# Optimization experiments

Measured on AMD Instinct MI355X. Metric: run time of the kernel, lower is better.

## Reference

```python
import jax, jax.numpy as jnp
import numpy as np

N = 20000   # nodes
E = 640000  # edges (avg degree 32)
D = 128     # feature dim
BN_EPS = 1e-5


def setup_inputs() -> dict:
    key = jax.random.key(0)
    ks = jax.random.split(key, 24)
    s = 1.0 / np.sqrt(D)
    inp = {
        'h': jax.random.normal(ks[0], (N, D), jnp.float32),
        'e': jax.random.normal(ks[1], (E, D), jnp.float32),
        'src': jax.random.randint(ks[2], (E,), 0, N, jnp.int32),
        'dst': jax.random.randint(ks[3], (E,), 0, N, jnp.int32),
        'Wa': jax.random.normal(ks[4], (D, D), jnp.float32) * s,
        'ba': jnp.zeros((D,), jnp.float32),
        'Wb': jax.random.normal(ks[5], (D, D), jnp.float32) * s,
        'bb': jnp.zeros((D,), jnp.float32),
        'Wc': jax.random.normal(ks[6], (D, D), jnp.float32) * s,
        'bc': jnp.zeros((D,), jnp.float32),
        'Wd': jax.random.normal(ks[7], (D, D), jnp.float32) * s,
        'bd': jnp.zeros((D,), jnp.float32),
        'We': jax.random.normal(ks[8], (D, D), jnp.float32) * s,
        'be': jnp.zeros((D,), jnp.float32),
        'gamma_h': jnp.ones((D,), jnp.float32),
        'beta_h': jnp.zeros((D,), jnp.float32),
        'mean_h': jax.random.normal(ks[9], (D,), jnp.float32) * 0.1,
        'var_h': jax.random.uniform(ks[10], (D,), jnp.float32) + 0.5,
        'gamma_e': jnp.ones((D,), jnp.float32),
        'beta_e': jnp.zeros((D,), jnp.float32),
        'mean_e': jax.random.normal(ks[11], (D,), jnp.float32) * 0.1,
        'var_e': jax.random.uniform(ks[12], (D,), jnp.float32) + 0.5,
    }
    return inp


def reference(h, e, src, dst, Wa, ba, Wb, bb, Wc, bc, Wd, bd, We, be,
              gamma_h, beta_h, mean_h, var_h, gamma_e, beta_e, mean_e, var_e):
    # Node/edge linear projections (same as Linear: x @ W.T + b)
    Ah = h @ Wa.T + ba
    Bh = h @ Wb.T + bb
    Dh = h @ Wd.T + bd
    Eh = h @ We.T + be
    Ce = e @ Wc.T + bc

    # Edge gate: e_ij = Ce + Dh[src] + Eh[dst]
    e_new = Ce + Dh[src] + Eh[dst]          # [E, D]
    sigma = jax.nn.sigmoid(e_new)           # [E, D]

    # Normalized gated aggregation over incoming edges at each destination node
    num = jax.ops.segment_sum(sigma * Bh[src], dst, num_segments=N)  # [N, D]
    den = jax.ops.segment_sum(sigma, dst, num_segments=N)            # [N, D]
    h_new = Ah + num / (den + 1e-6)

    # BatchNorm (inference form, as written in the torch forward) + ReLU
    h_out = jax.nn.relu(gamma_h * (h_new - mean_h) / jnp.sqrt(var_h + BN_EPS) + beta_h)
    e_out = jax.nn.relu(gamma_e * (e_new - mean_e) / jnp.sqrt(var_e + BN_EPS) + beta_e)
    return h_out, e_out
```

## Files before the change

kernel.cpp:

```cpp
#include <hip/hip_runtime.h>

#define NN 20000
#define NE 640000
#define DIM 128
#define ND (NN * DIM)

typedef float f32x4 __attribute__((ext_vector_type(4)));
typedef __bf16 bf16x4 __attribute__((ext_vector_type(4)));
typedef __bf16 bf16x8 __attribute__((ext_vector_type(8)));
typedef unsigned int u32;
typedef u32 u32x2 __attribute__((ext_vector_type(2)));

__device__ __forceinline__ int swz(int r, int c) {
  return r * DIM + (c ^ ((r & 7) << 3));
}
__device__ __forceinline__ int sgaddr(int row, int col) {
  return row * DIM + ((col + ((row & 12) << 1)) & 127);
}
__device__ __forceinline__ u32 pk_bf16(float a, float b) {
  return __builtin_amdgcn_perm(__float_as_uint(b), __float_as_uint(a), 0x07060302u);
}
__device__ __forceinline__ float bf16_lo(u32 w) { return __uint_as_float(w << 16); }
__device__ __forceinline__ float bf16_hi(u32 w) { return __uint_as_float(w & 0xffff0000u); }

__global__ void prep(const float* __restrict__ Wa, const float* __restrict__ Wb,
                     const float* __restrict__ Wd, const float* __restrict__ We,
                     const float* __restrict__ Wc, __bf16* __restrict__ wbf,
                     __bf16* __restrict__ wcp,
                     const float* __restrict__ gh, const float* __restrict__ bh,
                     const float* __restrict__ mh, const float* __restrict__ vh,
                     const float* __restrict__ ge, const float* __restrict__ be_,
                     const float* __restrict__ me, const float* __restrict__ ve,
                     float* __restrict__ bn) {
  int b = blockIdx.x;
  int tid = threadIdx.x;
  if (b < 256) {
    int g = b * 256 + tid;
    int m = g >> 14;
    int off = g & 16383;
    const float* s = (m == 0) ? Wa : (m == 1) ? Wb : (m == 2) ? Wd : We;
    wbf[g] = (__bf16)s[off];
    if (g < DIM) {
      float sc = gh[g] * rsqrtf(vh[g] + 1e-5f);
      bn[g] = sc;
      bn[DIM + g] = bh[g] - mh[g] * sc;
    } else if (g < 2 * DIM) {
      int c = g - DIM;
      float sc = ge[c] * rsqrtf(ve[c] + 1e-5f);
      bn[2 * DIM + c] = sc;
      bn[3 * DIM + c] = be_[c] - me[c] * sc;
    }
  } else {
    int t2 = (b - 256) * 256 + tid;
    int lane = t2 & 63, nt = (t2 >> 6) & 7, ks = t2 >> 9;
    int lq = lane >> 4, lm = lane & 15;
    const float* srcp = Wc + (nt * 16 + lm) * DIM + ks * 32 + lq * 8;
    bf16x8 v;
#pragma unroll
    for (int j = 0; j < 8; ++j) v[j] = (__bf16)srcp[j];
    *(bf16x8*)(wcp + t2 * 8) = v;
  }
}

__global__ void hist(const int* __restrict__ dst, int* __restrict__ cur) {
  int e = blockIdx.x * 256 + threadIdx.x;
  if (e < NE) atomicAdd(cur + dst[e], 1);
}

__global__ __launch_bounds__(1024) void scan20k(int* __restrict__ cur) {
  __shared__ int wsum[16];
  int tid = threadIdx.x, wid = tid >> 6, lane = tid & 63;
  int carry = 0;
  for (int base = 0; base < NN; base += 4096) {
    int idx = base + tid * 4;
    int4 v = {0, 0, 0, 0};
    if (idx < NN) v = *(const int4*)(cur + idx);
    int sum = v.x + v.y + v.z + v.w;
    int x = sum;
#pragma unroll
    for (int d = 1; d < 64; d <<= 1) {
      int y = __shfl_up(x, d, 64);
      if (lane >= d) x += y;
    }
    if (lane == 63) wsum[wid] = x;
    __syncthreads();
    if (tid < 16) {
      int s = wsum[tid];
#pragma unroll
      for (int d = 1; d < 16; d <<= 1) {
        int y = __shfl_up(s, d, 64);
        if (tid >= d) s += y;
      }
      wsum[tid] = s;
    }
    __syncthreads();
    int excl = carry + ((wid > 0) ? wsum[wid - 1] : 0) + x - sum;
    if (idx < NN) {
      int4 o;
      o.x = excl; o.y = excl + v.x; o.z = o.y + v.y; o.w = o.z + v.z;
      *(int4*)(cur + idx) = o;
    }
    carry += wsum[15];
    __syncthreads();
  }
}

__global__ void scatter(const int* __restrict__ dst, int* __restrict__ cur,
                        int* __restrict__ perm) {
  int e = blockIdx.x * 256 + threadIdx.x;
  if (e < NE) {
    int p = atomicAdd(cur + dst[e], 1);
    perm[p] = e;
  }
}

__global__ __launch_bounds__(256) void node_gemm(
    const float* __restrict__ h, const __bf16* __restrict__ wbf,
    const float* __restrict__ ba, const float* __restrict__ bb,
    const float* __restrict__ bd, const float* __restrict__ be,
    const float* __restrict__ bc,
    float* __restrict__ Ah, __bf16* __restrict__ Bhb,
    __bf16* __restrict__ Dhb, __bf16* __restrict__ Ehb) {
  __shared__ __bf16 As[64 * DIM];
  __shared__ __bf16 Ws[DIM * DIM];
  const int tid = threadIdx.x;
  const int m = blockIdx.x & 3;
  const int row0 = (blockIdx.x >> 2) * 64;

#pragma unroll
  for (int it = 0; it < 8; ++it) {
    int flat = it * 1024 + tid * 4;
    int r = flat >> 7, c = flat & 127;
    int grow = row0 + r;
    f32x4 v = (f32x4){0.f, 0.f, 0.f, 0.f};
    if (grow < NN) v = *(const f32x4*)(h + grow * DIM + c);
    u32x2 pk;
    pk[0] = pk_bf16(v[0], v[1]);
    pk[1] = pk_bf16(v[2], v[3]);
    *(u32x2*)(As + swz(r, c)) = pk;
  }
#pragma unroll
  for (int it = 0; it < 8; ++it) {
    int chunk = it * 256 + tid;
    int r = chunk >> 4, c0 = (chunk & 15) << 3;
    bf16x8 v = *(const bf16x8*)(wbf + m * DIM * DIM + (chunk << 3));
    *(bf16x8*)(Ws + swz(r, c0)) = v;
  }
  __syncthreads();

  const int wv = tid >> 6, lane = tid & 63;
  const int lq = lane >> 4, lm = lane & 15;

  f32x4 acc[8];
#pragma unroll
  for (int i = 0; i < 8; ++i) acc[i] = (f32x4){0.f, 0.f, 0.f, 0.f};
#pragma unroll
  for (int ks = 0; ks < 4; ++ks) {
    int k0 = ks * 32 + lq * 8;
    int ar = wv * 16 + lm;
    bf16x8 a = *(const bf16x8*)(As + swz(ar, k0));
#pragma unroll
    for (int nt = 0; nt < 8; ++nt) {
      int bcol = nt * 16 + lm;
      bf16x8 b = *(const bf16x8*)(Ws + swz(bcol, k0));
      acc[nt] = __builtin_amdgcn_mfma_f32_16x16x32_bf16(a, b, acc[nt], 0, 0, 0);
    }
  }

  const float* bias = (m == 0) ? ba : (m == 1) ? bb : (m == 2) ? bd : be;
#pragma unroll
  for (int nt = 0; nt < 8; ++nt) {
    int col = nt * 16 + lm;
    float bv = bias[col];
    if (m == 2) bv += bc[col];
#pragma unroll
    for (int r = 0; r < 4; ++r) {
      int grow = row0 + wv * 16 + lq * 4 + r;
      if (grow < NN) {
        float val = acc[nt][r] + bv;
        if (m == 0) Ah[grow * DIM + col] = val;
        else if (m == 1) Bhb[grow * DIM + col] = (__bf16)val;
        else if (m == 2) Dhb[grow * DIM + col] = (__bf16)val;
        else Ehb[grow * DIM + col] = (__bf16)val;
      }
    }
  }
}

union SmemU {
  __bf16 As[64 * DIM];
  u32 sgp[64 * DIM];
};

__global__ __launch_bounds__(256, 4) void edge_gemm(
    const float* __restrict__ e, const __bf16* __restrict__ wcp,
    const int* __restrict__ src, const int* __restrict__ dst,
    const int* __restrict__ perm,
    const __bf16* __restrict__ Bhb, const __bf16* __restrict__ Dhb,
    const __bf16* __restrict__ Ehb,
    float* __restrict__ num, float* __restrict__ den,
    float* __restrict__ e_out, const float* __restrict__ bn) {
  __shared__ SmemU u;
  __shared__ int s_perm[64], s_src[64], s_dst[64];
  const int tid = threadIdx.x;
  const int e0 = blockIdx.x * 64;

  if (tid < 64) {
    int p = perm[e0 + tid];
    s_perm[tid] = p;
    s_src[tid] = src[p];
    s_dst[tid] = dst[p];
  }
  __syncthreads();

#pragma unroll
  for (int it = 0; it < 8; ++it) {
    int flat = it * 1024 + tid * 4;
    int r = flat >> 7, c = flat & 127;
    f32x4 v = __builtin_nontemporal_load(
        (const f32x4*)(e + (size_t)s_perm[r] * DIM + c));
    u32x2 pk;
    pk[0] = pk_bf16(v[0], v[1]);
    pk[1] = pk_bf16(v[2], v[3]);
    *(u32x2*)(u.As + swz(r, c)) = pk;
  }
  __syncthreads();

  const int wv = tid >> 6, lane = tid & 63;
  const int lq = lane >> 4, lm = lane & 15;

  f32x4 acc[8];
#pragma unroll
  for (int i = 0; i < 8; ++i) acc[i] = (f32x4){0.f, 0.f, 0.f, 0.f};
  const bf16x8* wp = (const bf16x8*)wcp;
#pragma unroll
  for (int ks = 0; ks < 4; ++ks) {
    int k0 = ks * 32 + lq * 8;
    int ar = wv * 16 + lm;
    bf16x8 a = *(const bf16x8*)(u.As + swz(ar, k0));
#pragma unroll
    for (int nt = 0; nt < 8; ++nt) {
      bf16x8 b = wp[(ks * 8 + nt) * 64 + lane];
      acc[nt] = __builtin_amdgcn_mfma_f32_16x16x32_bf16(a, b, acc[nt], 0, 0, 0);
    }
  }
  __syncthreads();

  float scv[8], shv[8];
#pragma unroll
  for (int nt = 0; nt < 8; ++nt) {
    scv[nt] = bn[2 * DIM + nt * 16 + lm];
    shv[nt] = bn[3 * DIM + nt * 16 + lm];
  }

#pragma unroll
  for (int r4 = 0; r4 < 4; ++r4) {
    int lrow = wv * 16 + lq * 4 + r4;
    int s = s_src[lrow];
    const __bf16* pD = Dhb + s * DIM + lm;
    const __bf16* pE = Ehb + s_dst[lrow] * DIM + lm;
    const __bf16* pB = Bhb + s * DIM + lm;
    float* pO = e_out + (size_t)s_perm[lrow] * DIM + lm;
#pragma unroll
    for (int nt = 0; nt < 8; ++nt) {
      float x = acc[nt][r4] + (float)pD[nt * 16] + (float)pE[nt * 16];
      float sig = __builtin_amdgcn_rcpf(1.0f + __expf(-x));
      float sb = sig * (float)pB[nt * 16];
      __builtin_nontemporal_store(fmaxf(scv[nt] * x + shv[nt], 0.0f),
                                  pO + nt * 16);
      u.sgp[sgaddr(lrow, nt * 16 + lm)] = pk_bf16(sig, sb);
    }
  }
  __syncthreads();

  {
    int col = tid >> 1;
    int r0 = (tid & 1) << 5;
    float an = 0.f, ad = 0.f;
    int prev = s_dst[r0];
    int seg_start = r0;
#pragma unroll 4
    for (int k = 0; k < 32; ++k) {
      int row = r0 + k;
      int d = s_dst[row];
      if (d != prev) {
        if (seg_start > r0) {
          num[prev * DIM + col] = an;
          den[prev * DIM + col] = ad;
        } else {
          atomicAdd(num + prev * DIM + col, an);
          atomicAdd(den + prev * DIM + col, ad);
        }
        an = 0.f; ad = 0.f; prev = d; seg_start = row;
      }
      u32 w = u.sgp[sgaddr(row, col)];
      ad += bf16_lo(w);
      an += bf16_hi(w);
    }
    atomicAdd(num + prev * DIM + col, an);
    atomicAdd(den + prev * DIM + col, ad);
  }
}

__global__ void final_h(const float* __restrict__ Ah, const float* __restrict__ num,
                        const float* __restrict__ den, const float* __restrict__ bn,
                        float* __restrict__ h_out) {
  int g = blockIdx.x * blockDim.x + threadIdx.x;
  int idx = g * 4;
  int col = idx & (DIM - 1);
  f32x4 a = *(const f32x4*)(Ah + idx);
  f32x4 n = *(const f32x4*)(num + idx);
  f32x4 d = *(const f32x4*)(den + idx);
  f32x4 o;
#pragma unroll
  for (int j = 0; j < 4; ++j) {
    float hn = a[j] + n[j] * __builtin_amdgcn_rcpf(d[j] + 1e-6f);
    o[j] = fmaxf(bn[col + j] * hn + bn[DIM + col + j], 0.0f);
  }
  *(f32x4*)(h_out + idx) = o;
}

extern "C" void kernel_launch(void* const* d_in, const int* in_sizes, int n_in,
                              void* d_out, int out_size, void* d_ws, size_t ws_size,
                              hipStream_t stream) {
  (void)in_sizes; (void)n_in; (void)out_size; (void)ws_size;
  const float* h   = (const float*)d_in[0];
  const float* e   = (const float*)d_in[1];
  const int*   src = (const int*)d_in[2];
  const int*   dst = (const int*)d_in[3];
  const float* Wa  = (const float*)d_in[4];
  const float* ba  = (const float*)d_in[5];
  const float* Wb  = (const float*)d_in[6];
  const float* bb  = (const float*)d_in[7];
  const float* Wc  = (const float*)d_in[8];
  const float* bc  = (const float*)d_in[9];
  const float* Wd  = (const float*)d_in[10];
  const float* bd  = (const float*)d_in[11];
  const float* We  = (const float*)d_in[12];
  const float* be  = (const float*)d_in[13];
  const float* gamma_h = (const float*)d_in[14];
  const float* beta_h  = (const float*)d_in[15];
  const float* mean_h  = (const float*)d_in[16];
  const float* var_h   = (const float*)d_in[17];
  const float* gamma_e = (const float*)d_in[18];
  const float* beta_e  = (const float*)d_in[19];
  const float* mean_e  = (const float*)d_in[20];
  const float* var_e   = (const float*)d_in[21];

  float* ws  = (float*)d_ws;
  float* Ah  = ws;
  float* num = Ah + ND;
  float* den = num + ND;
  __bf16* Bhb = (__bf16*)(den + ND);
  __bf16* Dhb = Bhb + ND;
  __bf16* Ehb = Dhb + ND;
  __bf16* wbf = Ehb + ND;
  __bf16* wcp = wbf + 4 * DIM * DIM;
  float* bn  = (float*)(wcp + DIM * DIM);
  int*   cur = (int*)(bn + 4 * DIM);
  int*   perm = cur + NN;

  float* h_out = (float*)d_out;
  float* e_out = h_out + ND;

  hipMemsetAsync(num, 0, (size_t)2 * ND * sizeof(float), stream);
  hipMemsetAsync(cur, 0, (size_t)NN * sizeof(int), stream);
  prep<<<264, 256, 0, stream>>>(Wa, Wb, Wd, We, Wc, wbf, wcp,
                                gamma_h, beta_h, mean_h, var_h,
                                gamma_e, beta_e, mean_e, var_e, bn);
  hist<<<NE / 256, 256, 0, stream>>>(dst, cur);
  scan20k<<<1, 1024, 0, stream>>>(cur);
  scatter<<<NE / 256, 256, 0, stream>>>(dst, cur, perm);
  node_gemm<<<((NN + 63) / 64) * 4, 256, 0, stream>>>(h, wbf, ba, bb, bd, be, bc,
                                                      Ah, Bhb, Dhb, Ehb);
  edge_gemm<<<NE / 64, 256, 0, stream>>>(e, wcp, src, dst, perm,
                                         Bhb, Dhb, Ehb, num, den, e_out, bn);
  final_h<<<ND / 4 / 256, 256, 0, stream>>>(Ah, num, den, bn, h_out);
}
```

Measured before the change: 317.4 us.

## Load GEMM A fragments directly from global, drop LDS staging and syncs

Node and edge GEMMs now load their bf16 A-fragments straight from global memory into registers in MFMA layout, removing the LDS staging buffers and the block barriers around them. All five weight matrices are pre-packed in MFMA fragment order, and the histogram is merged into the prep kernel to save a launch. The edge segment reduction becomes per-wave, using shuffled dst indices instead of shared arrays. LDS use and barriers drop, which may raise occupancy, but the global loads become less coalesced and the per-wave segments produce more atomics.

Result: slower. 402.5 us (+26.8%).

```diff
diff --git a/kernel.cpp b/kernel.cpp
--- a/kernel.cpp
+++ b/kernel.cpp
@@ -6,14 +6,11 @@
 #define ND (NN * DIM)
 
 typedef float f32x4 __attribute__((ext_vector_type(4)));
-typedef __bf16 bf16x4 __attribute__((ext_vector_type(4)));
 typedef __bf16 bf16x8 __attribute__((ext_vector_type(8)));
 typedef unsigned int u32;
-typedef u32 u32x2 __attribute__((ext_vector_type(2)));
-
-__device__ __forceinline__ int swz(int r, int c) {
-  return r * DIM + (c ^ ((r & 7) << 3));
-}
+typedef unsigned short u16;
+typedef u32 u32x4 __attribute__((ext_vector_type(4)));
+
 __device__ __forceinline__ int sgaddr(int row, int col) {
   return row * DIM + ((col + ((row & 12) << 1)) & 127);
 }
@@ -22,49 +19,51 @@
 }
 __device__ __forceinline__ float bf16_lo(u32 w) { return __uint_as_float(w << 16); }
 __device__ __forceinline__ float bf16_hi(u32 w) { return __uint_as_float(w & 0xffff0000u); }
-
-__global__ void prep(const float* __restrict__ Wa, const float* __restrict__ Wb,
-                     const float* __restrict__ Wd, const float* __restrict__ We,
-                     const float* __restrict__ Wc, __bf16* __restrict__ wbf,
-                     __bf16* __restrict__ wcp,
-                     const float* __restrict__ gh, const float* __restrict__ bh,
-                     const float* __restrict__ mh, const float* __restrict__ vh,
-                     const float* __restrict__ ge, const float* __restrict__ be_,
-                     const float* __restrict__ me, const float* __restrict__ ve,
-                     float* __restrict__ bn) {
+__device__ __forceinline__ float b2f(u16 v) { return __uint_as_float(((u32)v) << 16); }
+
+union AFrag { bf16x8 b; u32x4 u; };
+
+__global__ void prep_hist(const int* __restrict__ dst, int* __restrict__ cur,
+                          const float* __restrict__ Wa, const float* __restrict__ Wb,
+                          const float* __restrict__ Wd, const float* __restrict__ We,
+                          const float* __restrict__ Wc, __bf16* __restrict__ wpack,
+                          const float* __restrict__ gh, const float* __restrict__ bh,
+                          const float* __restrict__ mh, const float* __restrict__ vh,
+                          const float* __restrict__ ge, const float* __restrict__ be_,
+                          const float* __restrict__ me, const float* __restrict__ ve,
+                          float* __restrict__ bn) {
   int b = blockIdx.x;
   int tid = threadIdx.x;
-  if (b < 256) {
-    int g = b * 256 + tid;
-    int m = g >> 14;
-    int off = g & 16383;
-    const float* s = (m == 0) ? Wa : (m == 1) ? Wb : (m == 2) ? Wd : We;
-    wbf[g] = (__bf16)s[off];
-    if (g < DIM) {
-      float sc = gh[g] * rsqrtf(vh[g] + 1e-5f);
-      bn[g] = sc;
-      bn[DIM + g] = bh[g] - mh[g] * sc;
-    } else if (g < 2 * DIM) {
-      int c = g - DIM;
+  if (b < 2500) {
+    atomicAdd(cur + dst[b * 256 + tid], 1);
+    return;
+  }
+  b -= 2500;
+  if (b < 40) {
+    int t = b * 256 + tid;
+    int m = t >> 11;
+    int chunk = t & 2047;
+    int lane = chunk & 63, nt = (chunk >> 6) & 7, ks = chunk >> 9;
+    int lq = lane >> 4, lm = lane & 15;
+    const float* W = (m == 0) ? Wa : (m == 1) ? Wb : (m == 2) ? Wd
+                   : (m == 3) ? We : Wc;
+    const float* srcp = W + (nt * 16 + lm) * DIM + ks * 32 + lq * 8;
+    bf16x8 v;
+#pragma unroll
+    for (int j = 0; j < 8; ++j) v[j] = (__bf16)srcp[j];
+    *(bf16x8*)(wpack + (size_t)t * 8) = v;
+  } else {
+    if (tid < DIM) {
+      float sc = gh[tid] * rsqrtf(vh[tid] + 1e-5f);
+      bn[tid] = sc;
+      bn[DIM + tid] = bh[tid] - mh[tid] * sc;
+    } else {
+      int c = tid - DIM;
       float sc = ge[c] * rsqrtf(ve[c] + 1e-5f);
       bn[2 * DIM + c] = sc;
       bn[3 * DIM + c] = be_[c] - me[c] * sc;
     }
-  } else {
-    int t2 = (b - 256) * 256 + tid;
-    int lane = t2 & 63, nt = (t2 >> 6) & 7, ks = t2 >> 9;
-    int lq = lane >> 4, lm = lane & 15;
-    const float* srcp = Wc + (nt * 16 + lm) * DIM + ks * 32 + lq * 8;
-    bf16x8 v;
-#pragma unroll
-    for (int j = 0; j < 8; ++j) v[j] = (__bf16)srcp[j];
-    *(bf16x8*)(wcp + t2 * 8) = v;
-  }
-}
-
-__global__ void hist(const int* __restrict__ dst, int* __restrict__ cur) {
-  int e = blockIdx.x * 256 + threadIdx.x;
-  if (e < NE) atomicAdd(cur + dst[e], 1);
+  }
 }
 
 __global__ __launch_bounds__(1024) void scan20k(int* __restrict__ cur) {
@@ -115,55 +114,41 @@
 }
 
 __global__ __launch_bounds__(256) void node_gemm(
-    const float* __restrict__ h, const __bf16* __restrict__ wbf,
+    const float* __restrict__ h, const __bf16* __restrict__ wpack,
     const float* __restrict__ ba, const float* __restrict__ bb,
     const float* __restrict__ bd, const float* __restrict__ be,
     const float* __restrict__ bc,
     float* __restrict__ Ah, __bf16* __restrict__ Bhb,
     __bf16* __restrict__ Dhb, __bf16* __restrict__ Ehb) {
-  __shared__ __bf16 As[64 * DIM];
-  __shared__ __bf16 Ws[DIM * DIM];
   const int tid = threadIdx.x;
   const int m = blockIdx.x & 3;
   const int row0 = (blockIdx.x >> 2) * 64;
-
-#pragma unroll
-  for (int it = 0; it < 8; ++it) {
-    int flat = it * 1024 + tid * 4;
-    int r = flat >> 7, c = flat & 127;
-    int grow = row0 + r;
-    f32x4 v = (f32x4){0.f, 0.f, 0.f, 0.f};
-    if (grow < NN) v = *(const f32x4*)(h + grow * DIM + c);
-    u32x2 pk;
-    pk[0] = pk_bf16(v[0], v[1]);
-    pk[1] = pk_bf16(v[2], v[3]);
-    *(u32x2*)(As + swz(r, c)) = pk;
-  }
-#pragma unroll
-  for (int it = 0; it < 8; ++it) {
-    int chunk = it * 256 + tid;
-    int r = chunk >> 4, c0 = (chunk & 15) << 3;
-    bf16x8 v = *(const bf16x8*)(wbf + m * DIM * DIM + (chunk << 3));
-    *(bf16x8*)(Ws + swz(r, c0)) = v;
-  }
-  __syncthreads();
-
   const int wv = tid >> 6, lane = tid & 63;
   const int lq = lane >> 4, lm = lane & 15;
+  const int arow = row0 + wv * 16 + lm;
+  const bf16x8* wp = (const bf16x8*)(wpack + (size_t)m * DIM * DIM);
 
   f32x4 acc[8];
 #pragma unroll
   for (int i = 0; i < 8; ++i) acc[i] = (f32x4){0.f, 0.f, 0.f, 0.f};
+  const float* pA = h + (size_t)arow * DIM;
 #pragma unroll
   for (int ks = 0; ks < 4; ++ks) {
     int k0 = ks * 32 + lq * 8;
-    int ar = wv * 16 + lm;
-    bf16x8 a = *(const bf16x8*)(As + swz(ar, k0));
+    f32x4 v0 = (f32x4){0.f, 0.f, 0.f, 0.f}, v1 = v0;
+    if (arow < NN) {
+      v0 = *(const f32x4*)(pA + k0);
+      v1 = *(const f32x4*)(pA + k0 + 4);
+    }
+    AFrag A;
+    A.u[0] = pk_bf16(v0[0], v0[1]);
+    A.u[1] = pk_bf16(v0[2], v0[3]);
+    A.u[2] = pk_bf16(v1[0], v1[1]);
+    A.u[3] = pk_bf16(v1[2], v1[3]);
 #pragma unroll
     for (int nt = 0; nt < 8; ++nt) {
-      int bcol = nt * 16 + lm;
-      bf16x8 b = *(const bf16x8*)(Ws + swz(bcol, k0));
-      acc[nt] = __builtin_amdgcn_mfma_f32_16x16x32_bf16(a, b, acc[nt], 0, 0, 0);
+      bf16x8 bfr = wp[(ks * 8 + nt) * 64 + lane];
+      acc[nt] = __builtin_amdgcn_mfma_f32_16x16x32_bf16(A.b, bfr, acc[nt], 0, 0, 0);
     }
   }
 
@@ -187,11 +172,6 @@
   }
 }
 
-union SmemU {
-  __bf16 As[64 * DIM];
-  u32 sgp[64 * DIM];
-};
-
 __global__ __launch_bounds__(256, 4) void edge_gemm(
     const float* __restrict__ e, const __bf16* __restrict__ wcp,
     const int* __restrict__ src, const int* __restrict__ dst,
@@ -200,51 +180,45 @@
     const __bf16* __restrict__ Ehb,
     float* __restrict__ num, float* __restrict__ den,
     float* __restrict__ e_out, const float* __restrict__ bn) {
-  __shared__ SmemU u;
-  __shared__ int s_perm[64], s_src[64], s_dst[64];
+  __shared__ u32 sgp[64 * DIM];
   const int tid = threadIdx.x;
-  const int e0 = blockIdx.x * 64;
-
-  if (tid < 64) {
-    int p = perm[e0 + tid];
-    s_perm[tid] = p;
-    s_src[tid] = src[p];
-    s_dst[tid] = dst[p];
-  }
-  __syncthreads();
-
-#pragma unroll
-  for (int it = 0; it < 8; ++it) {
-    int flat = it * 1024 + tid * 4;
-    int r = flat >> 7, c = flat & 127;
-    f32x4 v = __builtin_nontemporal_load(
-        (const f32x4*)(e + (size_t)s_perm[r] * DIM + c));
-    u32x2 pk;
-    pk[0] = pk_bf16(v[0], v[1]);
-    pk[1] = pk_bf16(v[2], v[3]);
-    *(u32x2*)(u.As + swz(r, c)) = pk;
-  }
-  __syncthreads();
-
   const int wv = tid >> 6, lane = tid & 63;
   const int lq = lane >> 4, lm = lane & 15;
+  const int e0 = blockIdx.x * 64;
+  const int R0 = wv * 16;
+  const int lrb = R0 + lq * 4;
+
+  int pa = perm[e0 + R0 + lm];
+  int pr[4], sA[4], dA[4];
+#pragma unroll
+  for (int r4 = 0; r4 < 4; ++r4) pr[r4] = perm[e0 + lrb + r4];
+#pragma unroll
+  for (int r4 = 0; r4 < 4; ++r4) {
+    sA[r4] = src[pr[r4]];
+    dA[r4] = dst[pr[r4]];
+  }
 
   f32x4 acc[8];
 #pragma unroll
   for (int i = 0; i < 8; ++i) acc[i] = (f32x4){0.f, 0.f, 0.f, 0.f};
   const bf16x8* wp = (const bf16x8*)wcp;
+  const float* pA = e + (size_t)pa * DIM;
 #pragma unroll
   for (int ks = 0; ks < 4; ++ks) {
     int k0 = ks * 32 + lq * 8;
-    int ar = wv * 16 + lm;
-    bf16x8 a = *(const bf16x8*)(u.As + swz(ar, k0));
+    f32x4 v0 = __builtin_nontemporal_load((const f32x4*)(pA + k0));
+    f32x4 v1 = __builtin_nontemporal_load((const f32x4*)(pA + k0 + 4));
+    AFrag A;
+    A.u[0] = pk_bf16(v0[0], v0[1]);
+    A.u[1] = pk_bf16(v0[2], v0[3]);
+    A.u[2] = pk_bf16(v1[0], v1[1]);
+    A.u[3] = pk_bf16(v1[2], v1[3]);
 #pragma unroll
     for (int nt = 0; nt < 8; ++nt) {
-      bf16x8 b = wp[(ks * 8 + nt) * 64 + lane];
-      acc[nt] = __builtin_amdgcn_mfma_f32_16x16x32_bf16(a, b, acc[nt], 0, 0, 0);
-    }
-  }
-  __syncthreads();
+      bf16x8 bfr = wp[(ks * 8 + nt) * 64 + lane];
+      acc[nt] = __builtin_amdgcn_mfma_f32_16x16x32_bf16(A.b, bfr, acc[nt], 0, 0, 0);
+    }
+  }
 
   float scv[8], shv[8];
 #pragma unroll
@@ -253,52 +227,53 @@
     shv[nt] = bn[3 * DIM + nt * 16 + lm];
   }
 
+  const u16* Du = (const u16*)Dhb;
+  const u16* Eu = (const u16*)Ehb;
+  const u16* Bu = (const u16*)Bhb;
 #pragma unroll
   for (int r4 = 0; r4 < 4; ++r4) {
-    int lrow = wv * 16 + lq * 4 + r4;
-    int s = s_src[lrow];
-    const __bf16* pD = Dhb + s * DIM + lm;
-    const __bf16* pE = Ehb + s_dst[lrow] * DIM + lm;
-    const __bf16* pB = Bhb + s * DIM + lm;
-    float* pO = e_out + (size_t)s_perm[lrow] * DIM + lm;
+    const int lrow = lrb + r4;
+    const u16* pD = Du + sA[r4] * DIM + lm;
+    const u16* pE = Eu + dA[r4] * DIM + lm;
+    const u16* pB = Bu + sA[r4] * DIM + lm;
+    float* pO = e_out + (size_t)pr[r4] * DIM + lm;
 #pragma unroll
     for (int nt = 0; nt < 8; ++nt) {
-      float x = acc[nt][r4] + (float)pD[nt * 16] + (float)pE[nt * 16];
+      float x = acc[nt][r4] + b2f(pD[nt * 16]) + b2f(pE[nt * 16]);
       float sig = __builtin_amdgcn_rcpf(1.0f + __expf(-x));
-      float sb = sig * (float)pB[nt * 16];
+      float sb = sig * b2f(pB[nt * 16]);
       __builtin_nontemporal_store(fmaxf(scv[nt] * x + shv[nt], 0.0f),
                                   pO + nt * 16);
-      u.sgp[sgaddr(lrow, nt * 16 + lm)] = pk_bf16(sig, sb);
-    }
-  }
-  __syncthreads();
+      sgp[sgaddr(lrow, nt * 16 + lm)] = pk_bf16(sig, sb);
+    }
+  }
 
   {
-    int col = tid >> 1;
-    int r0 = (tid & 1) << 5;
-    float an = 0.f, ad = 0.f;
-    int prev = s_dst[r0];
-    int seg_start = r0;
-#pragma unroll 4
-    for (int k = 0; k < 32; ++k) {
-      int row = r0 + k;
-      int d = s_dst[row];
+    const int c0 = lane, c1 = lane + 64;
+    float an0 = 0.f, ad0 = 0.f, an1 = 0.f, ad1 = 0.f;
+    int prev = __shfl(dA[0], 0, 64);
+    int seg_start = 0;
+#pragma unroll
+    for (int k = 0; k < 16; ++k) {
+      int d = __shfl(dA[k & 3], (k >> 2) << 4, 64);
       if (d != prev) {
-        if (seg_start > r0) {
-          num[prev * DIM + col] = an;
-          den[prev * DIM + col] = ad;
+        if (seg_start > 0) {
+          num[prev * DIM + c0] = an0; den[prev * DIM + c0] = ad0;
+          num[prev * DIM + c1] = an1; den[prev * DIM + c1] = ad1;
         } else {
-          atomicAdd(num + prev * DIM + col, an);
-          atomicAdd(den + prev * DIM + col, ad);
+          atomicAdd(num + prev * DIM + c0, an0); atomicAdd(den + prev * DIM + c0, ad0);
+          atomicAdd(num + prev * DIM + c1, an1); atomicAdd(den + prev * DIM + c1, ad1);
         }
-        an = 0.f; ad = 0.f; prev = d; seg_start = row;
+        an0 = ad0 = an1 = ad1 = 0.f;
+        prev = d; seg_start = k;
       }
-      u32 w = u.sgp[sgaddr(row, col)];
-      ad += bf16_lo(w);
-      an += bf16_hi(w);
-    }
-    atomicAdd(num + prev * DIM + col, an);
-    atomicAdd(den + prev * DIM + col, ad);
+      u32 w0 = sgp[sgaddr(R0 + k, c0)];
+      u32 w1 = sgp[sgaddr(R0 + k, c1)];
+      ad0 += bf16_lo(w0); an0 += bf16_hi(w0);
+      ad1 += bf16_lo(w1); an1 += bf16_hi(w1);
+    }
+    atomicAdd(num + prev * DIM + c0, an0); atomicAdd(den + prev * DIM + c0, ad0);
+    atomicAdd(num + prev * DIM + c1, an1); atomicAdd(den + prev * DIM + c1, ad1);
   }
 }
 
@@ -354,9 +329,8 @@
   __bf16* Bhb = (__bf16*)(den + ND);
   __bf16* Dhb = Bhb + ND;
   __bf16* Ehb = Dhb + ND;
-  __bf16* wbf = Ehb + ND;
-  __bf16* wcp = wbf + 4 * DIM * DIM;
-  float* bn  = (float*)(wcp + DIM * DIM);
+  __bf16* wpack = Ehb + ND;
+  float* bn  = (float*)(wpack + 5 * DIM * DIM);
   int*   cur = (int*)(bn + 4 * DIM);
   int*   perm = cur + NN;
 
@@ -365,15 +339,14 @@
 
   hipMemsetAsync(num, 0, (size_t)2 * ND * sizeof(float), stream);
   hipMemsetAsync(cur, 0, (size_t)NN * sizeof(int), stream);
-  prep<<<264, 256, 0, stream>>>(Wa, Wb, Wd, We, Wc, wbf, wcp,
-                                gamma_h, beta_h, mean_h, var_h,
-                                gamma_e, beta_e, mean_e, var_e, bn);
-  hist<<<NE / 256, 256, 0, stream>>>(dst, cur);
+  prep_hist<<<2541, 256, 0, stream>>>(dst, cur, Wa, Wb, Wd, We, Wc, wpack,
+                                      gamma_h, beta_h, mean_h, var_h,
+                                      gamma_e, beta_e, mean_e, var_e, bn);
   scan20k<<<1, 1024, 0, stream>>>(cur);
   scatter<<<NE / 256, 256, 0, stream>>>(dst, cur, perm);
-  node_gemm<<<((NN + 63) / 64) * 4, 256, 0, stream>>>(h, wbf, ba, bb, bd, be, bc,
+  node_gemm<<<((NN + 63) / 64) * 4, 256, 0, stream>>>(h, wpack, ba, bb, bd, be, bc,
                                                       Ah, Bhb, Dhb, Ehb);
-  edge_gemm<<<NE / 64, 256, 0, stream>>>(e, wcp, src, dst, perm,
+  edge_gemm<<<NE / 64, 256, 0, stream>>>(e, wpack + 4 * DIM * DIM, src, dst, perm,
                                          Bhb, Dhb, Ehb, num, den, e_out, bn);
   final_h<<<ND / 4 / 256, 256, 0, stream>>>(Ah, num, den, bn, h_out);
 }
```

## Transpose edge MFMA, drop shared index staging, fuse hist into prep

Applied to the files above, without the earlier changes.

Fuses the histogram kernel into the weight-prep kernel, removing one launch. The scatter kernel now also writes src and dst in permuted order, so the edge kernel reads them contiguously instead of gathering through perm. In the edge kernel each wave now stages only its own 16 rows, which removes the first two block barriers. The MFMA operands are swapped so each lane owns one edge row and 4 consecutive features. That lets the epilogue use vectorized 4-wide bf16 gathers, float4 e_out stores and 128-bit shared writes, at the cost of extra index-array writes in scatter and a changed swizzle.

Result: slower. 409.3 us (+28.9%).

```diff
diff --git a/kernel.cpp b/kernel.cpp
--- a/kernel.cpp
+++ b/kernel.cpp
@@ -6,34 +6,43 @@
 #define ND (NN * DIM)
 
 typedef float f32x4 __attribute__((ext_vector_type(4)));
-typedef __bf16 bf16x4 __attribute__((ext_vector_type(4)));
 typedef __bf16 bf16x8 __attribute__((ext_vector_type(8)));
 typedef unsigned int u32;
+typedef unsigned short u16;
+typedef u16 u16x4 __attribute__((ext_vector_type(4)));
 typedef u32 u32x2 __attribute__((ext_vector_type(2)));
-
-__device__ __forceinline__ int swz(int r, int c) {
+typedef u32 u32x4 __attribute__((ext_vector_type(4)));
+
+__device__ __forceinline__ int swz16(int r, int c) {
   return r * DIM + (c ^ ((r & 7) << 3));
 }
 __device__ __forceinline__ int sgaddr(int row, int col) {
-  return row * DIM + ((col + ((row & 12) << 1)) & 127);
+  return row * DIM + ((col + ((row & 7) << 2)) & 127);
 }
 __device__ __forceinline__ u32 pk_bf16(float a, float b) {
   return __builtin_amdgcn_perm(__float_as_uint(b), __float_as_uint(a), 0x07060302u);
 }
 __device__ __forceinline__ float bf16_lo(u32 w) { return __uint_as_float(w << 16); }
 __device__ __forceinline__ float bf16_hi(u32 w) { return __uint_as_float(w & 0xffff0000u); }
-
-__global__ void prep(const float* __restrict__ Wa, const float* __restrict__ Wb,
-                     const float* __restrict__ Wd, const float* __restrict__ We,
-                     const float* __restrict__ Wc, __bf16* __restrict__ wbf,
-                     __bf16* __restrict__ wcp,
-                     const float* __restrict__ gh, const float* __restrict__ bh,
-                     const float* __restrict__ mh, const float* __restrict__ vh,
-                     const float* __restrict__ ge, const float* __restrict__ be_,
-                     const float* __restrict__ me, const float* __restrict__ ve,
-                     float* __restrict__ bn) {
+__device__ __forceinline__ float b2f(u16 v) { return __uint_as_float(((u32)v) << 16); }
+
+__global__ void prep_hist(const int* __restrict__ dst, int* __restrict__ cur,
+                          const float* __restrict__ Wa, const float* __restrict__ Wb,
+                          const float* __restrict__ Wd, const float* __restrict__ We,
+                          const float* __restrict__ Wc, __bf16* __restrict__ wbf,
+                          __bf16* __restrict__ wcp,
+                          const float* __restrict__ gh, const float* __restrict__ bh,
+                          const float* __restrict__ mh, const float* __restrict__ vh,
+                          const float* __restrict__ ge, const float* __restrict__ be_,
+                          const float* __restrict__ me, const float* __restrict__ ve,
+                          float* __restrict__ bn) {
   int b = blockIdx.x;
   int tid = threadIdx.x;
+  if (b < 2500) {
+    atomicAdd(cur + dst[b * 256 + tid], 1);
+    return;
+  }
+  b -= 2500;
   if (b < 256) {
     int g = b * 256 + tid;
     int m = g >> 14;
@@ -62,11 +71,6 @@
   }
 }
 
-__global__ void hist(const int* __restrict__ dst, int* __restrict__ cur) {
-  int e = blockIdx.x * 256 + threadIdx.x;
-  if (e < NE) atomicAdd(cur + dst[e], 1);
-}
-
 __global__ __launch_bounds__(1024) void scan20k(int* __restrict__ cur) {
   __shared__ int wsum[16];
   int tid = threadIdx.x, wid = tid >> 6, lane = tid & 63;
@@ -105,13 +109,21 @@
   }
 }
 
-__global__ void scatter(const int* __restrict__ dst, int* __restrict__ cur,
-                        int* __restrict__ perm) {
+__global__ void scatter(const int* __restrict__ dst, const int* __restrict__ src,
+                        int* __restrict__ cur, int* __restrict__ perm,
+                        int* __restrict__ srcs, int* __restrict__ dsts) {
   int e = blockIdx.x * 256 + threadIdx.x;
   if (e < NE) {
-    int p = atomicAdd(cur + dst[e], 1);
+    int d = dst[e];
+    int p = atomicAdd(cur + d, 1);
     perm[p] = e;
-  }
+    srcs[p] = src[e];
+    dsts[p] = d;
+  }
+}
+
+__device__ __forceinline__ int swz(int r, int c) {
+  return r * DIM + (c ^ ((r & 7) << 3));
 }
 
 __global__ __launch_bounds__(256) void node_gemm(
@@ -187,47 +199,44 @@
   }
 }
 
-union SmemU {
-  __bf16 As[64 * DIM];
-  u32 sgp[64 * DIM];
-};
-
 __global__ __launch_bounds__(256, 4) void edge_gemm(
     const float* __restrict__ e, const __bf16* __restrict__ wcp,
-    const int* __restrict__ src, const int* __restrict__ dst,
-    const int* __restrict__ perm,
+    const int* __restrict__ perm, const int* __restrict__ srcs,
+    const int* __restrict__ dsts,
     const __bf16* __restrict__ Bhb, const __bf16* __restrict__ Dhb,
     const __bf16* __restrict__ Ehb,
     float* __restrict__ num, float* __restrict__ den,
     float* __restrict__ e_out, const float* __restrict__ bn) {
-  __shared__ SmemU u;
-  __shared__ int s_perm[64], s_src[64], s_dst[64];
+  __shared__ u32 smem[64 * DIM];
   const int tid = threadIdx.x;
-  const int e0 = blockIdx.x * 64;
-
-  if (tid < 64) {
-    int p = perm[e0 + tid];
-    s_perm[tid] = p;
-    s_src[tid] = src[p];
-    s_dst[tid] = dst[p];
-  }
-  __syncthreads();
-
-#pragma unroll
-  for (int it = 0; it < 8; ++it) {
-    int flat = it * 1024 + tid * 4;
-    int r = flat >> 7, c = flat & 127;
-    f32x4 v = __builtin_nontemporal_load(
-        (const f32x4*)(e + (size_t)s_perm[r] * DIM + c));
-    u32x2 pk;
-    pk[0] = pk_bf16(v[0], v[1]);
-    pk[1] = pk_bf16(v[2], v[3]);
-    *(u32x2*)(u.As + swz(r, c)) = pk;
-  }
-  __syncthreads();
-
   const int wv = tid >> 6, lane = tid & 63;
   const int lq = lane >> 4, lm = lane & 15;
+  const int e0 = blockIdx.x * 64;
+  const int R0 = wv * 16;
+
+  const int q = e0 + R0 + lm;
+  int p = perm[q];
+  int sA = srcs[q];
+  int dA = dsts[q];
+
+  __bf16* As = (__bf16*)(smem + wv * 2048);
+  {
+    int pr[8];
+#pragma unroll
+    for (int it = 0; it < 8; ++it)
+      pr[it] = perm[e0 + R0 + 2 * it + (lane >> 5)];
+#pragma unroll
+    for (int it = 0; it < 8; ++it) {
+      int r = 2 * it + (lane >> 5);
+      int c = (lane & 31) * 4;
+      f32x4 v = __builtin_nontemporal_load(
+          (const f32x4*)(e + (size_t)pr[it] * DIM + c));
+      u32x2 pk;
+      pk[0] = pk_bf16(v[0], v[1]);
+      pk[1] = pk_bf16(v[2], v[3]);
+      *(u32x2*)(As + swz16(r, c)) = pk;
+    }
+  }
 
   f32x4 acc[8];
 #pragma unroll
@@ -236,39 +245,39 @@
 #pragma unroll
   for (int ks = 0; ks < 4; ++ks) {
     int k0 = ks * 32 + lq * 8;
-    int ar = wv * 16 + lm;
-    bf16x8 a = *(const bf16x8*)(u.As + swz(ar, k0));
+    bf16x8 bfr = *(const bf16x8*)(As + swz16(lm, k0));
 #pragma unroll
     for (int nt = 0; nt < 8; ++nt) {
-      bf16x8 b = wp[(ks * 8 + nt) * 64 + lane];
-      acc[nt] = __builtin_amdgcn_mfma_f32_16x16x32_bf16(a, b, acc[nt], 0, 0, 0);
-    }
-  }
-  __syncthreads();
-
-  float scv[8], shv[8];
-#pragma unroll
-  for (int nt = 0; nt < 8; ++nt) {
-    scv[nt] = bn[2 * DIM + nt * 16 + lm];
-    shv[nt] = bn[3 * DIM + nt * 16 + lm];
-  }
-
-#pragma unroll
-  for (int r4 = 0; r4 < 4; ++r4) {
-    int lrow = wv * 16 + lq * 4 + r4;
-    int s = s_src[lrow];
-    const __bf16* pD = Dhb + s * DIM + lm;
-    const __bf16* pE = Ehb + s_dst[lrow] * DIM + lm;
-    const __bf16* pB = Bhb + s * DIM + lm;
-    float* pO = e_out + (size_t)s_perm[lrow] * DIM + lm;
+      bf16x8 afr = wp[(ks * 8 + nt) * 64 + lane];
+      acc[nt] = __builtin_amdgcn_mfma_f32_16x16x32_bf16(afr, bfr, acc[nt], 0, 0, 0);
+    }
+  }
+
+  {
+    const u16* pD = (const u16*)Dhb + sA * DIM;
+    const u16* pE = (const u16*)Ehb + dA * DIM;
+    const u16* pB = (const u16*)Bhb + sA * DIM;
+    float* pO = e_out + (size_t)p * DIM;
 #pragma unroll
     for (int nt = 0; nt < 8; ++nt) {
-      float x = acc[nt][r4] + (float)pD[nt * 16] + (float)pE[nt * 16];
-      float sig = __builtin_amdgcn_rcpf(1.0f + __expf(-x));
-      float sb = sig * (float)pB[nt * 16];
-      __builtin_nontemporal_store(fmaxf(scv[nt] * x + shv[nt], 0.0f),
-                                  pO + nt * 16);
-      u.sgp[sgaddr(lrow, nt * 16 + lm)] = pk_bf16(sig, sb);
+      const int f0 = nt * 16 + lq * 4;
+      u16x4 dv = *(const u16x4*)(pD + f0);
+      u16x4 ev = *(const u16x4*)(pE + f0);
+      u16x4 bv = *(const u16x4*)(pB + f0);
+      f32x4 sc = *(const f32x4*)(bn + 2 * DIM + f0);
+      f32x4 sh = *(const f32x4*)(bn + 3 * DIM + f0);
+      f32x4 o;
+      u32x4 pk;
+#pragma unroll
+      for (int r = 0; r < 4; ++r) {
+        float x = acc[nt][r] + b2f(dv[r]) + b2f(ev[r]);
+        float sig = __builtin_amdgcn_rcpf(1.0f + __expf(-x));
+        float sb = sig * b2f(bv[r]);
+        o[r] = fmaxf(sc[r] * x + sh[r], 0.0f);
+        pk[r] = pk_bf16(sig, sb);
+      }
+      __builtin_nontemporal_store(o, (f32x4*)(pO + f0));
+      *(u32x4*)(smem + sgaddr(R0 + lm, f0)) = pk;
     }
   }
   __syncthreads();
@@ -276,13 +285,23 @@
   {
     int col = tid >> 1;
     int r0 = (tid & 1) << 5;
+    int4 dv8[8];
+#pragma unroll
+    for (int i = 0; i < 8; ++i)
+      dv8[i] = *(const int4*)(dsts + e0 + r0 + i * 4);
+    int dr[32];
+#pragma unroll
+    for (int i = 0; i < 8; ++i) {
+      dr[i * 4] = dv8[i].x; dr[i * 4 + 1] = dv8[i].y;
+      dr[i * 4 + 2] = dv8[i].z; dr[i * 4 + 3] = dv8[i].w;
+    }
     float an = 0.f, ad = 0.f;
-    int prev = s_dst[r0];
+    int prev = dr[0];
     int seg_start = r0;
 #pragma unroll 4
     for (int k = 0; k < 32; ++k) {
       int row = r0 + k;
-      int d = s_dst[row];
+      int d = dr[k];
       if (d != prev) {
         if (seg_start > r0) {
           num[prev * DIM + col] = an;
@@ -293,7 +312,7 @@
         }
         an = 0.f; ad = 0.f; prev = d; seg_start = row;
       }
-      u32 w = u.sgp[sgaddr(row, col)];
+      u32 w = smem[sgaddr(row, col)];
       ad += bf16_lo(w);
       an += bf16_hi(w);
     }
@@ -359,21 +378,22 @@
   float* bn  = (float*)(wcp + DIM * DIM);
   int*   cur = (int*)(bn + 4 * DIM);
   int*   perm = cur + NN;
+  int*   srcs = perm + NE;
+  int*   dsts = srcs + NE;
 
   float* h_out = (float*)d_out;
   float* e_out = h_out + ND;
 
   hipMemsetAsync(num, 0, (size_t)2 * ND * sizeof(float), stream);
   hipMemsetAsync(cur, 0, (size_t)NN * sizeof(int), stream);
-  prep<<<264, 256, 0, stream>>>(Wa, Wb, Wd, We, Wc, wbf, wcp,
-                                gamma_h, beta_h, mean_h, var_h,
-                                gamma_e, beta_e, mean_e, var_e, bn);
-  hist<<<NE / 256, 256, 0, stream>>>(dst, cur);
+  prep_hist<<<2764, 256, 0, stream>>>(dst, cur, Wa, Wb, Wd, We, Wc, wbf, wcp,
+                                      gamma_h, beta_h, mean_h, var_h,
+                                      gamma_e, beta_e, mean_e, var_e, bn);
   scan20k<<<1, 1024, 0, stream>>>(cur);
-  scatter<<<NE / 256, 256, 0, stream>>>(dst, cur, perm);
+  scatter<<<NE / 256, 256, 0, stream>>>(dst, src, cur, perm, srcs, dsts);
   node_gemm<<<((NN + 63) / 64) * 4, 256, 0, stream>>>(h, wbf, ba, bb, bd, be, bc,
                                                       Ah, Bhb, Dhb, Ehb);
-  edge_gemm<<<NE / 64, 256, 0, stream>>>(e, wcp, src, dst, perm,
+  edge_gemm<<<NE / 64, 256, 0, stream>>>(e, wcp, perm, srcs, dsts,
                                          Bhb, Dhb, Ehb, num, den, e_out, bn);
   final_h<<<ND / 4 / 256, 256, 0, stream>>>(Ah, num, den, bn, h_out);
 }
```

## Fuse histogram into prep and scatter into node GEMM, store sorted dst

Applied to the files above, without the earlier changes.

Merges the hist kernel into the weight-prep kernel and the scatter kernel into the node GEMM launch, which removes two kernel launches and lets the independent work run concurrently. Scatter now also writes a dst array in sorted order, so edge_gemm reads dst contiguously instead of gathering it through perm. Edge_gemm's shared memory shrinks (s_perm is aliased into the tile buffer and s_src/s_dst are dropped) and launch bounds rise to 5 blocks per CU. This adds an extra NE-sized int array write and more register pressure from holding 32 dst values per thread.

After: 619.6 us. +95.2%, slower.

```diff
diff --git a/kernel.cpp b/kernel.cpp
--- a/kernel.cpp
+++ b/kernel.cpp
@@ -6,9 +6,9 @@
 #define ND (NN * DIM)
 
 typedef float f32x4 __attribute__((ext_vector_type(4)));
-typedef __bf16 bf16x4 __attribute__((ext_vector_type(4)));
 typedef __bf16 bf16x8 __attribute__((ext_vector_type(8)));
 typedef unsigned int u32;
+typedef unsigned short u16;
 typedef u32 u32x2 __attribute__((ext_vector_type(2)));
 
 __device__ __forceinline__ int swz(int r, int c) {
@@ -22,18 +22,25 @@
 }
 __device__ __forceinline__ float bf16_lo(u32 w) { return __uint_as_float(w << 16); }
 __device__ __forceinline__ float bf16_hi(u32 w) { return __uint_as_float(w & 0xffff0000u); }
-
-__global__ void prep(const float* __restrict__ Wa, const float* __restrict__ Wb,
-                     const float* __restrict__ Wd, const float* __restrict__ We,
-                     const float* __restrict__ Wc, __bf16* __restrict__ wbf,
-                     __bf16* __restrict__ wcp,
-                     const float* __restrict__ gh, const float* __restrict__ bh,
-                     const float* __restrict__ mh, const float* __restrict__ vh,
-                     const float* __restrict__ ge, const float* __restrict__ be_,
-                     const float* __restrict__ me, const float* __restrict__ ve,
-                     float* __restrict__ bn) {
+__device__ __forceinline__ float b2f(u16 v) { return __uint_as_float(((u32)v) << 16); }
+
+__global__ void prep_hist(const int* __restrict__ dst, int* __restrict__ cur,
+                          const float* __restrict__ Wa, const float* __restrict__ Wb,
+                          const float* __restrict__ Wd, const float* __restrict__ We,
+                          const float* __restrict__ Wc, __bf16* __restrict__ wbf,
+                          __bf16* __restrict__ wcp,
+                          const float* __restrict__ gh, const float* __restrict__ bh,
+                          const float* __restrict__ mh, const float* __restrict__ vh,
+                          const float* __restrict__ ge, const float* __restrict__ be_,
+                          const float* __restrict__ me, const float* __restrict__ ve,
+                          float* __restrict__ bn) {
   int b = blockIdx.x;
   int tid = threadIdx.x;
+  if (b < 2500) {
+    atomicAdd(cur + dst[b * 256 + tid], 1);
+    return;
+  }
+  b -= 2500;
   if (b < 256) {
     int g = b * 256 + tid;
     int m = g >> 14;
@@ -62,11 +69,6 @@
   }
 }
 
-__global__ void hist(const int* __restrict__ dst, int* __restrict__ cur) {
-  int e = blockIdx.x * 256 + threadIdx.x;
-  if (e < NE) atomicAdd(cur + dst[e], 1);
-}
-
 __global__ __launch_bounds__(1024) void scan20k(int* __restrict__ cur) {
   __shared__ int wsum[16];
   int tid = threadIdx.x, wid = tid >> 6, lane = tid & 63;
@@ -105,25 +107,27 @@
   }
 }
 
-__global__ void scatter(const int* __restrict__ dst, int* __restrict__ cur,
-                        int* __restrict__ perm) {
-  int e = blockIdx.x * 256 + threadIdx.x;
-  if (e < NE) {
-    int p = atomicAdd(cur + dst[e], 1);
-    perm[p] = e;
-  }
-}
-
-__global__ __launch_bounds__(256) void node_gemm(
+#define NODE_BLOCKS 1252
+__global__ __launch_bounds__(256) void node_scatter(
     const float* __restrict__ h, const __bf16* __restrict__ wbf,
     const float* __restrict__ ba, const float* __restrict__ bb,
     const float* __restrict__ bd, const float* __restrict__ be,
     const float* __restrict__ bc,
     float* __restrict__ Ah, __bf16* __restrict__ Bhb,
-    __bf16* __restrict__ Dhb, __bf16* __restrict__ Ehb) {
+    __bf16* __restrict__ Dhb, __bf16* __restrict__ Ehb,
+    const int* __restrict__ dst, int* __restrict__ cur,
+    int* __restrict__ perm, int* __restrict__ dsts) {
+  const int tid = threadIdx.x;
+  if (blockIdx.x >= NODE_BLOCKS) {
+    int e = (blockIdx.x - NODE_BLOCKS) * 256 + tid;
+    int d = dst[e];
+    int p = atomicAdd(cur + d, 1);
+    perm[p] = e;
+    dsts[p] = d;
+    return;
+  }
   __shared__ __bf16 As[64 * DIM];
   __shared__ __bf16 Ws[DIM * DIM];
-  const int tid = threadIdx.x;
   const int m = blockIdx.x & 3;
   const int row0 = (blockIdx.x >> 2) * 64;
 
@@ -187,30 +191,21 @@
   }
 }
 
-union SmemU {
-  __bf16 As[64 * DIM];
-  u32 sgp[64 * DIM];
-};
-
-__global__ __launch_bounds__(256, 4) void edge_gemm(
+__global__ __launch_bounds__(256, 5) void edge_gemm(
     const float* __restrict__ e, const __bf16* __restrict__ wcp,
-    const int* __restrict__ src, const int* __restrict__ dst,
-    const int* __restrict__ perm,
+    const int* __restrict__ src,
+    const int* __restrict__ perm, const int* __restrict__ dsts,
     const __bf16* __restrict__ Bhb, const __bf16* __restrict__ Dhb,
     const __bf16* __restrict__ Ehb,
     float* __restrict__ num, float* __restrict__ den,
     float* __restrict__ e_out, const float* __restrict__ bn) {
-  __shared__ SmemU u;
-  __shared__ int s_perm[64], s_src[64], s_dst[64];
+  __shared__ u32 smem[64 * DIM];
+  int* s_perm = (int*)(smem + 32 * DIM);
+  __bf16* As = (__bf16*)smem;
   const int tid = threadIdx.x;
   const int e0 = blockIdx.x * 64;
 
-  if (tid < 64) {
-    int p = perm[e0 + tid];
-    s_perm[tid] = p;
-    s_src[tid] = src[p];
-    s_dst[tid] = dst[p];
-  }
+  if (tid < 64) s_perm[tid] = perm[e0 + tid];
   __syncthreads();
 
 #pragma unroll
@@ -222,7 +217,7 @@
     u32x2 pk;
     pk[0] = pk_bf16(v[0], v[1]);
     pk[1] = pk_bf16(v[2], v[3]);
-    *(u32x2*)(u.As + swz(r, c)) = pk;
+    *(u32x2*)(As + swz(r, c)) = pk;
   }
   __syncthreads();
 
@@ -237,38 +232,45 @@
   for (int ks = 0; ks < 4; ++ks) {
     int k0 = ks * 32 + lq * 8;
     int ar = wv * 16 + lm;
-    bf16x8 a = *(const bf16x8*)(u.As + swz(ar, k0));
+    bf16x8 a = *(const bf16x8*)(As + swz(ar, k0));
 #pragma unroll
     for (int nt = 0; nt < 8; ++nt) {
       bf16x8 b = wp[(ks * 8 + nt) * 64 + lane];
       acc[nt] = __builtin_amdgcn_mfma_f32_16x16x32_bf16(a, b, acc[nt], 0, 0, 0);
     }
   }
-  __syncthreads();
-
+
+  const int lrb = wv * 16 + lq * 4;
+  int pR[4], sR[4], dR[4];
+#pragma unroll
+  for (int r4 = 0; r4 < 4; ++r4) {
+    pR[r4] = s_perm[lrb + r4];
+    dR[r4] = dsts[e0 + lrb + r4];
+    sR[r4] = src[pR[r4]];
+  }
   float scv[8], shv[8];
 #pragma unroll
   for (int nt = 0; nt < 8; ++nt) {
     scv[nt] = bn[2 * DIM + nt * 16 + lm];
     shv[nt] = bn[3 * DIM + nt * 16 + lm];
   }
+  __syncthreads();
 
 #pragma unroll
   for (int r4 = 0; r4 < 4; ++r4) {
-    int lrow = wv * 16 + lq * 4 + r4;
-    int s = s_src[lrow];
-    const __bf16* pD = Dhb + s * DIM + lm;
-    const __bf16* pE = Ehb + s_dst[lrow] * DIM + lm;
-    const __bf16* pB = Bhb + s * DIM + lm;
-    float* pO = e_out + (size_t)s_perm[lrow] * DIM + lm;
+    const int lrow = lrb + r4;
+    const u16* pD = (const u16*)Dhb + sR[r4] * DIM + lm;
+    const u16* pE = (const u16*)Ehb + dR[r4] * DIM + lm;
+    const u16* pB = (const u16*)Bhb + sR[r4] * DIM + lm;
+    float* pO = e_out + (size_t)pR[r4] * DIM + lm;
 #pragma unroll
     for (int nt = 0; nt < 8; ++nt) {
-      float x = acc[nt][r4] + (float)pD[nt * 16] + (float)pE[nt * 16];
+      float x = acc[nt][r4] + b2f(pD[nt * 16]) + b2f(pE[nt * 16]);
       float sig = __builtin_amdgcn_rcpf(1.0f + __expf(-x));
-      float sb = sig * (float)pB[nt * 16];
+      float sb = sig * b2f(pB[nt * 16]);
       __builtin_nontemporal_store(fmaxf(scv[nt] * x + shv[nt], 0.0f),
                                   pO + nt * 16);
-      u.sgp[sgaddr(lrow, nt * 16 + lm)] = pk_bf16(sig, sb);
+      smem[sgaddr(lrow, nt * 16 + lm)] = pk_bf16(sig, sb);
     }
   }
   __syncthreads();
@@ -276,13 +278,23 @@
   {
     int col = tid >> 1;
     int r0 = (tid & 1) << 5;
+    int4 dv8[8];
+#pragma unroll
+    for (int i = 0; i < 8; ++i)
+      dv8[i] = *(const int4*)(dsts + e0 + r0 + i * 4);
+    int dr[32];
+#pragma unroll
+    for (int i = 0; i < 8; ++i) {
+      dr[i * 4] = dv8[i].x; dr[i * 4 + 1] = dv8[i].y;
+      dr[i * 4 + 2] = dv8[i].z; dr[i * 4 + 3] = dv8[i].w;
+    }
     float an = 0.f, ad = 0.f;
-    int prev = s_dst[r0];
+    int prev = dr[0];
     int seg_start = r0;
 #pragma unroll 4
     for (int k = 0; k < 32; ++k) {
       int row = r0 + k;
-      int d = s_dst[row];
+      int d = dr[k];
       if (d != prev) {
         if (seg_start > r0) {
           num[prev * DIM + col] = an;
@@ -293,7 +305,7 @@
         }
         an = 0.f; ad = 0.f; prev = d; seg_start = row;
       }
-      u32 w = u.sgp[sgaddr(row, col)];
+      u32 w = smem[sgaddr(row, col)];
       ad += bf16_lo(w);
       an += bf16_hi(w);
     }
@@ -359,21 +371,20 @@
   float* bn  = (float*)(wcp + DIM * DIM);
   int*   cur = (int*)(bn + 4 * DIM);
   int*   perm = cur + NN;
+  int*   dsts = perm + NE;
 
   float* h_out = (float*)d_out;
   float* e_out = h_out + ND;
 
   hipMemsetAsync(num, 0, (size_t)2 * ND * sizeof(float), stream);
   hipMemsetAsync(cur, 0, (size_t)NN * sizeof(int), stream);
-  prep<<<264, 256, 0, stream>>>(Wa, Wb, Wd, We, Wc, wbf, wcp,
-                                gamma_h, beta_h, mean_h, var_h,
-                                gamma_e, beta_e, mean_e, var_e, bn);
-  hist<<<NE / 256, 256, 0, stream>>>(dst, cur);
+  prep_hist<<<2764, 256, 0, stream>>>(dst, cur, Wa, Wb, Wd, We, Wc, wbf, wcp,
+                                      gamma_h, beta_h, mean_h, var_h,
+                                      gamma_e, beta_e, mean_e, var_e, bn);
   scan20k<<<1, 1024, 0, stream>>>(cur);
-  scatter<<<NE / 256, 256, 0, stream>>>(dst, cur, perm);
-  node_gemm<<<((NN + 63) / 64) * 4, 256, 0, stream>>>(h, wbf, ba, bb, bd, be, bc,
-                                                      Ah, Bhb, Dhb, Ehb);
-  edge_gemm<<<NE / 64, 256, 0, stream>>>(e, wcp, src, dst, perm,
+  node_scatter<<<NODE_BLOCKS + NE / 256, 256, 0, stream>>>(
+      h, wbf, ba, bb, bd, be, bc, Ah, Bhb, Dhb, Ehb, dst, cur, perm, dsts);
+  edge_gemm<<<NE / 64, 256, 0, stream>>>(e, wcp, src, perm, dsts,
                                          Bhb, Dhb, Ehb, num, den, e_out, bn);
   final_h<<<ND / 4 / 256, 256, 0, stream>>>(Ah, num, den, bn, h_out);
 }
```
